# Kernel tuning notes

Measured on AMD Instinct MI355X. Metric: run time of the kernel, lower is better.

## Reference

```python
import jax, jax.numpy as jnp
import numpy as np

D_MODEL, D_HIDDEN, D_OUTPUT = 512, 1024, 128

def setup_inputs() -> dict:
    key = jax.random.key(0)
    ks = jax.random.split(key, 6)
    enc = jax.random.normal(ks[0], (8, 256, D_MODEL), dtype=jnp.float32)
    dec = jax.random.normal(ks[1], (8, 64, D_MODEL), dtype=jnp.float32)
    s1 = 1.0 / np.sqrt(2 * D_MODEL)
    s2 = 1.0 / np.sqrt(D_HIDDEN)
    W1 = jax.random.uniform(ks[2], (2 * D_MODEL, D_HIDDEN), jnp.float32, -s1, s1)
    b1 = jax.random.uniform(ks[3], (D_HIDDEN,), jnp.float32, -s1, s1)
    W2 = jax.random.uniform(ks[4], (D_HIDDEN, D_OUTPUT), jnp.float32, -s2, s2)
    b2 = jax.random.uniform(ks[5], (D_OUTPUT,), jnp.float32, -s2, s2)
    return {"encoder_state": enc, "decoder_state": dec, "W1": W1, "b1": b1, "W2": W2, "b2": b2}

def reference(encoder_state, decoder_state, W1, b1, W2, b2):
    # Split first linear's weight into encoder/decoder halves: equivalent to
    # concat([enc, dec], -1) @ W1, but avoids materializing the (B,T,U,2d) tensor.
    W_enc, W_dec = W1[:D_MODEL], W1[D_MODEL:]
    enc_proj = jnp.einsum('btd,dh->bth', encoder_state, W_enc)   # (B,T,H)
    dec_proj = jnp.einsum('bud,dh->buh', decoder_state, W_dec)   # (B,U,H)
    hidden = jnp.tanh(enc_proj[:, :, None, :] + dec_proj[:, None, :, :] + b1)  # (B,T,U,H)
    out = jnp.einsum('btuh,ho->btuo', hidden, W2) + b2           # (B,T,U,O)
    return out
```

## Files before the change

### kernel.cpp

```cpp
#include <hip/hip_runtime.h>
#include <hip/hip_bf16.h>


typedef _Float16 f16x8 __attribute__((ext_vector_type(8)));
typedef _Float16 f16x2 __attribute__((ext_vector_type(2)));
typedef float    f32x4 __attribute__((ext_vector_type(4)));

#define C2L 2.8853900817779268f

__device__ __forceinline__ float fast_exp2(float x) { return __builtin_amdgcn_exp2f(x); }

__device__ __forceinline__ f16x2 pk_cvt(float x, float y) {
    auto r = __builtin_amdgcn_cvt_pkrtz(x, y);
    union { decltype(r) a; f16x2 b; } c; c.a = r; return c.b;
}

__device__ __forceinline__ f16x8 tanh8(f16x8 e, f16x8 d) {
    const f16x8 one = {1,1,1,1,1,1,1,1};
    const f16x8 two = {2,2,2,2,2,2,2,2};
    const f16x8 cap = {126,126,126,126,126,126,126,126};
    union { f16x8 v; _Float16 s[8]; } p, r;
    p.v = e * d + one;
    p.v = __builtin_elementwise_min(p.v, cap);
    #pragma unroll
    for (int i = 0; i < 4; ++i) {
        _Float16 q  = p.s[2*i] * p.s[2*i+1];
        _Float16 rq = __builtin_amdgcn_rcph(q);
        r.s[2*i]   = p.s[2*i+1] * rq;
        r.s[2*i+1] = p.s[2*i]   * rq;
    }
    return one - two * r.v;
}

__device__ __forceinline__ void stage16(const void* g, void* l) {
    __builtin_amdgcn_global_load_lds(
        (const __attribute__((address_space(1))) unsigned int*)g,
        (__attribute__((address_space(3))) unsigned int*)l, 16, 0, 0);
}

__global__ __launch_bounds__(1024) void transpose_both(
    const float* __restrict__ W1, const float* __restrict__ W2,
    _Float16* __restrict__ W1T, _Float16* __restrict__ W2T)
{
    __shared__ float tile[32][33];
    int bx = blockIdx.x;
    const float* src; _Float16* dst; int C, c0;
    if (bx < 32) { src = W1; dst = W1T; C = 1024; c0 = bx * 32; }
    else         { src = W2; dst = W2T; C = 128;  c0 = (bx - 32) * 32; }
    int r0 = blockIdx.y * 32;
    int tx = threadIdx.x, ty = threadIdx.y;
    tile[ty][tx] = src[(r0 + ty) * C + (c0 + tx)];
    __syncthreads();
    dst[(size_t)(c0 + ty) * 1024 + (r0 + tx)] = (_Float16)tile[tx][ty];
}

__global__ __launch_bounds__(256) void proj_exp(
    const float* __restrict__ enc,
    const float* __restrict__ dec,
    const _Float16* __restrict__ W1T,
    const float* __restrict__ b1,
    _Float16* __restrict__ Ep,
    _Float16* __restrict__ Dp)
{
    const int K = 512;
    int tid  = threadIdx.x;
    int w    = tid >> 6, lane = tid & 63;
    int quad = lane >> 4, l15 = lane & 15;
    int m_base = blockIdx.y * 64 + w * 16;
    int n_base = blockIdx.x * 64;

    bool is_enc = (m_base < 2048);
    const float* A = is_enc ? (enc + (size_t)(m_base + l15) * K)
                            : (dec + (size_t)(m_base - 2048 + l15) * K);
    int koff = is_enc ? 0 : 512;

    f32x4 acc[4] = {};
    for (int kc = 0; kc < K; kc += 32) {
        int k = kc + quad * 8;
        float4 a_lo = *reinterpret_cast<const float4*>(A + k);
        float4 a_hi = *reinterpret_cast<const float4*>(A + k + 4);
        union { f16x8 v; f16x2 h[4]; } a;
        a.h[0] = pk_cvt(a_lo.x, a_lo.y);
        a.h[1] = pk_cvt(a_lo.z, a_lo.w);
        a.h[2] = pk_cvt(a_hi.x, a_hi.y);
        a.h[3] = pk_cvt(a_hi.z, a_hi.w);
        #pragma unroll
        for (int f = 0; f < 4; ++f) {
            int n = n_base + f * 16 + l15;
            f16x8 b = *reinterpret_cast<const f16x8*>(W1T + n * 1024 + koff + k);
            acc[f] = __builtin_amdgcn_mfma_f32_16x16x32_f16(a.v, b, acc[f], 0, 0, 0);
        }
    }

    #pragma unroll
    for (int f = 0; f < 4; ++f) {
        int col = n_base + f * 16 + l15;
        float bv = is_enc ? b1[col] : 0.0f;
        #pragma unroll
        for (int v = 0; v < 4; ++v) {
            int row = m_base + quad * 4 + v;
            float val = fast_exp2(C2L * (acc[f][v] + bv));
            if (is_enc) Ep[(size_t)row * 1024 + col] = (_Float16)val;
            else        Dp[(size_t)(row - 2048) * 1024 + col] = (_Float16)val;
        }
    }
}

__global__ __launch_bounds__(256, 2) void joint_main(
    const _Float16* __restrict__ Ep,
    const _Float16* __restrict__ Dp,
    const _Float16* __restrict__ W2T,
    const float* __restrict__ b2,
    float* __restrict__ out)
{
    __shared__ _Float16 sB[2][128 * 64];
    __shared__ _Float16 sE[4 * 1024];

    int t0 = blockIdx.x * 4, b = blockIdx.y;
    int tid  = threadIdx.x;
    int w    = tid >> 6, lane = tid & 63;
    int quad = lane >> 4, l15 = lane & 15;
    int u0   = w * 16;

    const _Float16* epB = Ep + (size_t)(b * 256 + t0) * 1024;
    const _Float16* dpr = Dp + (size_t)(b * 64 + u0 + l15) * 1024;

    f32x4 acc[4][8] = {};

    #pragma unroll
    for (int i = 0; i < 2; ++i) {
        int c = i * 256 + tid;
        stage16(epB + c * 8, sE + (i * 256 + (tid & 0xC0)) * 8);
    }
    #pragma unroll
    for (int i = 0; i < 4; ++i) {
        int c = i * 256 + tid;
        int row = c >> 3, kcs = c & 7;
        stage16(W2T + row * 1024 + ((kcs ^ (row & 7)) << 3),
                &sB[0][(i * 256 + (tid & 0xC0)) * 8]);
    }

    for (int it = 0; it < 16; ++it) {
        __syncthreads();
        if (it < 15) {
            int kb = (it + 1) * 64;
            _Float16* dst = sB[(it + 1) & 1];
            #pragma unroll
            for (int i = 0; i < 4; ++i) {
                int c = i * 256 + tid;
                int row = c >> 3, kcs = c & 7;
                stage16(W2T + row * 1024 + kb + ((kcs ^ (row & 7)) << 3),
                        dst + (i * 256 + (tid & 0xC0)) * 8);
            }
        }
        const _Float16* sb = sB[it & 1];
        #pragma unroll
        for (int ki2 = 0; ki2 < 2; ++ki2) {
            int k = it * 64 + ki2 * 32 + quad * 8;
            f16x8 d8 = *reinterpret_cast<const f16x8*>(dpr + k);
            f16x8 A[4];
            #pragma unroll
            for (int tt = 0; tt < 4; ++tt) {
                f16x8 e = *reinterpret_cast<const f16x8*>(sE + tt * 1024 + k);
                A[tt] = tanh8(e, d8);
            }
            int kc3 = ki2 * 4 + quad;
            int sw  = (kc3 ^ (l15 & 7)) << 3;
            #pragma unroll
            for (int f = 0; f < 8; ++f) {
                f16x8 bb = *reinterpret_cast<const f16x8*>(
                    sb + (f * 16 + l15) * 64 + sw);
                #pragma unroll
                for (int tt = 0; tt < 4; ++tt)
                    acc[tt][f] = __builtin_amdgcn_mfma_f32_16x16x32_f16(A[tt], bb, acc[tt][f], 0, 0, 0);
            }
        }
    }

    #pragma unroll
    for (int tt = 0; tt < 4; ++tt) {
        float* o = out + (size_t)(b * 256 + t0 + tt) * 64 * 128;
        #pragma unroll
        for (int f = 0; f < 8; ++f) {
            int oc = f * 16 + l15;
            float bv = b2[oc];
            #pragma unroll
            for (int v = 0; v < 4; ++v) {
                int u = u0 + quad * 4 + v;
                o[u * 128 + oc] = acc[tt][f][v] + bv;
            }
        }
    }
}

extern "C" void kernel_launch(void* const* d_in, const int* in_sizes, int n_in,
                              void* d_out, int out_size, void* d_ws, size_t ws_size,
                              hipStream_t stream) {
    const float* enc = (const float*)d_in[0];
    const float* dec = (const float*)d_in[1];
    const float* W1  = (const float*)d_in[2];
    const float* b1  = (const float*)d_in[3];
    const float* W2  = (const float*)d_in[4];
    const float* b2  = (const float*)d_in[5];
    float* out = (float*)d_out;

    char* ws = (char*)d_ws;
    _Float16* W1T = (_Float16*)(ws);
    _Float16* W2T = (_Float16*)(ws + (2u << 20));
    _Float16* EpP = (_Float16*)(ws + (2u << 20) + (256u << 10));
    _Float16* DpP = (_Float16*)(ws + (6u << 20) + (256u << 10));

    transpose_both<<<dim3(36, 32), dim3(32, 32), 0, stream>>>(W1, W2, W1T, W2T);

    proj_exp<<<dim3(16, 40), 256, 0, stream>>>(enc, dec, W1T, b1, EpP, DpP);

    joint_main<<<dim3(64, 8), 256, 0, stream>>>(EpP, DpP, W2T, b2, out);
}
```

Before: 155.9 us.

## Stage W1T tiles in LDS with double buffering and prefetch A in proj_exp

The projection kernel now loads 64x64 fp16 weight tiles into swizzled, double-buffered LDS with async global-to-LDS copies that all four waves share. It also register-prefetches the next chunk of fp32 activations while the current chunk runs through MFMA. This replaces direct per-wave global loads of W1T, which were redundant across waves and sat on the critical path. It adds a barrier each iteration and uses more LDS and registers, with launch bounds set to two blocks per CU.

```diff
diff --git a/kernel.cpp b/kernel.cpp
--- a/kernel.cpp
+++ b/kernel.cpp
@@ -54,7 +54,7 @@
     dst[(size_t)(c0 + ty) * 1024 + (r0 + tx)] = (_Float16)tile[tx][ty];
 }
 
-__global__ __launch_bounds__(256) void proj_exp(
+__global__ __launch_bounds__(256, 2) void proj_exp(
     const float* __restrict__ enc,
     const float* __restrict__ dec,
     const _Float16* __restrict__ W1T,
@@ -62,34 +62,81 @@
     _Float16* __restrict__ Ep,
     _Float16* __restrict__ Dp)
 {
+    __shared__ _Float16 sB[2][64 * 64];
+
     const int K = 512;
     int tid  = threadIdx.x;
     int w    = tid >> 6, lane = tid & 63;
     int quad = lane >> 4, l15 = lane & 15;
-    int m_base = blockIdx.y * 64 + w * 16;
+    int m_base = blockIdx.y * 64;
     int n_base = blockIdx.x * 64;
 
     bool is_enc = (m_base < 2048);
-    const float* A = is_enc ? (enc + (size_t)(m_base + l15) * K)
-                            : (dec + (size_t)(m_base - 2048 + l15) * K);
-    int koff = is_enc ? 0 : 512;
+    int row = m_base + w * 16 + l15;
+    const float* A = is_enc ? (enc + (size_t)row * K)
+                            : (dec + (size_t)(row - 2048) * K);
+    const _Float16* Bsrc = W1T + (is_enc ? 0 : 512);
 
     f32x4 acc[4] = {};
-    for (int kc = 0; kc < K; kc += 32) {
-        int k = kc + quad * 8;
-        float4 a_lo = *reinterpret_cast<const float4*>(A + k);
-        float4 a_hi = *reinterpret_cast<const float4*>(A + k + 4);
-        union { f16x8 v; f16x2 h[4]; } a;
-        a.h[0] = pk_cvt(a_lo.x, a_lo.y);
-        a.h[1] = pk_cvt(a_lo.z, a_lo.w);
-        a.h[2] = pk_cvt(a_hi.x, a_hi.y);
-        a.h[3] = pk_cvt(a_hi.z, a_hi.w);
-        #pragma unroll
-        for (int f = 0; f < 4; ++f) {
-            int n = n_base + f * 16 + l15;
-            f16x8 b = *reinterpret_cast<const f16x8*>(W1T + n * 1024 + koff + k);
-            acc[f] = __builtin_amdgcn_mfma_f32_16x16x32_f16(a.v, b, acc[f], 0, 0, 0);
-        }
+
+    #pragma unroll
+    for (int i = 0; i < 2; ++i) {
+        int c = i * 256 + tid;
+        int r = c >> 3, kcs = c & 7;
+        stage16(Bsrc + (size_t)(n_base + r) * 1024 + ((kcs ^ (r & 7)) << 3),
+                &sB[0][(i * 256 + (tid & 0xC0)) * 8]);
+    }
+    float4 a0lo = *reinterpret_cast<const float4*>(A + quad * 8);
+    float4 a0hi = *reinterpret_cast<const float4*>(A + quad * 8 + 4);
+    float4 a1lo = *reinterpret_cast<const float4*>(A + 32 + quad * 8);
+    float4 a1hi = *reinterpret_cast<const float4*>(A + 32 + quad * 8 + 4);
+
+    for (int it = 0; it < 8; ++it) {
+        __syncthreads();
+        float4 n0lo, n0hi, n1lo, n1hi;
+        if (it < 7) {
+            int kb = (it + 1) * 64;
+            _Float16* dst = sB[(it + 1) & 1];
+            #pragma unroll
+            for (int i = 0; i < 2; ++i) {
+                int c = i * 256 + tid;
+                int r = c >> 3, kcs = c & 7;
+                stage16(Bsrc + (size_t)(n_base + r) * 1024 + kb + ((kcs ^ (r & 7)) << 3),
+                        dst + (i * 256 + (tid & 0xC0)) * 8);
+            }
+            n0lo = *reinterpret_cast<const float4*>(A + kb + quad * 8);
+            n0hi = *reinterpret_cast<const float4*>(A + kb + quad * 8 + 4);
+            n1lo = *reinterpret_cast<const float4*>(A + kb + 32 + quad * 8);
+            n1hi = *reinterpret_cast<const float4*>(A + kb + 32 + quad * 8 + 4);
+        }
+        const _Float16* sb = sB[it & 1];
+        {
+            union { f16x8 v; f16x2 h[4]; } a;
+            a.h[0] = pk_cvt(a0lo.x, a0lo.y);
+            a.h[1] = pk_cvt(a0lo.z, a0lo.w);
+            a.h[2] = pk_cvt(a0hi.x, a0hi.y);
+            a.h[3] = pk_cvt(a0hi.z, a0hi.w);
+            int sw = ((0 * 4 + quad) ^ (l15 & 7)) << 3;
+            #pragma unroll
+            for (int f = 0; f < 4; ++f) {
+                f16x8 bb = *reinterpret_cast<const f16x8*>(sb + (f * 16 + l15) * 64 + sw);
+                acc[f] = __builtin_amdgcn_mfma_f32_16x16x32_f16(a.v, bb, acc[f], 0, 0, 0);
+            }
+        }
+        {
+            union { f16x8 v; f16x2 h[4]; } a;
+            a.h[0] = pk_cvt(a1lo.x, a1lo.y);
+            a.h[1] = pk_cvt(a1lo.z, a1lo.w);
+            a.h[2] = pk_cvt(a1hi.x, a1hi.y);
+            a.h[3] = pk_cvt(a1hi.z, a1hi.w);
+            int sw = ((1 * 4 + quad) ^ (l15 & 7)) << 3;
+            #pragma unroll
+            for (int f = 0; f < 4; ++f) {
+                f16x8 bb = *reinterpret_cast<const f16x8*>(sb + (f * 16 + l15) * 64 + sw);
+                acc[f] = __builtin_amdgcn_mfma_f32_16x16x32_f16(a.v, bb, acc[f], 0, 0, 0);
+            }
+        }
+        a0lo = n0lo; a0hi = n0hi; a1lo = n1lo; a1hi = n1hi;
     }
 
     #pragma unroll
@@ -98,10 +145,10 @@
         float bv = is_enc ? b1[col] : 0.0f;
         #pragma unroll
         for (int v = 0; v < 4; ++v) {
-            int row = m_base + quad * 4 + v;
+            int orow = m_base + w * 16 + quad * 4 + v;
             float val = fast_exp2(C2L * (acc[f][v] + bv));
-            if (is_enc) Ep[(size_t)row * 1024 + col] = (_Float16)val;
-            else        Dp[(size_t)(row - 2048) * 1024 + col] = (_Float16)val;
+            if (is_enc) Ep[(size_t)orow * 1024 + col] = (_Float16)val;
+            else        Dp[(size_t)(orow - 2048) * 1024 + col] = (_Float16)val;
         }
     }
 }
```

Result: faster. 138.4 us (-11.2%).
